# Optimization experiments

Measured on AMD Instinct MI355X. Metric: run time of the kernel, lower is better.

## Reference

```python
import jax, jax.numpy as jnp
import numpy as np

N_NODES = 50000
N_EDGES = 800000
H = 64  # n_hid


def _linear_params(key, fan_in, fan_out):
    lim = 1.0 / np.sqrt(fan_in)
    kw, kb = jax.random.split(key)
    w = jax.random.uniform(kw, (fan_in, fan_out), minval=-lim, maxval=lim, dtype=jnp.float32)
    b = jax.random.uniform(kb, (fan_out,), minval=-lim, maxval=lim, dtype=jnp.float32)
    return w, b


def setup_inputs() -> dict:
    key = jax.random.key(0)
    ks = jax.random.split(key, 10)
    nf_gc = jax.random.normal(ks[0], (N_NODES, H), dtype=jnp.float32)
    src = jax.random.randint(ks[1], (N_EDGES,), 0, N_NODES, dtype=jnp.int32)
    dst = jax.random.randint(ks[2], (N_EDGES,), 0, N_NODES, dtype=jnp.int32)
    res_w1, res_b1 = _linear_params(ks[3], H, H)
    res_w2, res_b2 = _linear_params(ks[4], H, H)
    lin1_w, lin1_b = _linear_params(ks[5], H, H)
    lin2_w, lin2_b = _linear_params(ks[6], H, H)
    msg_w1, msg_b1 = _linear_params(ks[7], 2 * H, 2 * H)
    msg_w2, msg_b2 = _linear_params(ks[8], 2 * H, 2 * H + 1)
    red_w, red_b = _linear_params(ks[9], 3 * H, H)
    return {
        'nf_gc': nf_gc, 'src': src, 'dst': dst,
        'res_w1': res_w1, 'res_b1': res_b1, 'res_w2': res_w2, 'res_b2': res_b2,
        'lin1_w': lin1_w, 'lin1_b': lin1_b, 'lin2_w': lin2_w, 'lin2_b': lin2_b,
        'msg_w1': msg_w1, 'msg_b1': msg_b1, 'msg_w2': msg_w2, 'msg_b2': msg_b2,
        'red_w': red_w, 'red_b': red_b,
    }


def reference(nf_gc, src, dst, res_w1, res_b1, res_w2, res_b2,
              lin1_w, lin1_b, lin2_w, lin2_b,
              msg_w1, msg_b1, msg_w2, msg_b2, red_w, red_b):
    n = nf_gc.shape[0]
    h = lin1_w.shape[0]
    # Residual block: lin2(lin1(x)) + x (no activation)
    x = ((nf_gc @ res_w1 + res_b1) @ res_w2 + res_b2) + nf_gc
    x1 = x @ lin1_w + lin1_b
    # Edge message: concat(src feat, dst feat) -> MLP(2h -> 2h -> 2h+1)
    e = jnp.concatenate([x[src], x[dst]], axis=1)          # [E, 2h]
    hmid = jax.nn.leaky_relu(e @ msg_w1 + msg_b1, 0.2)     # [E, 2h]
    o = hmid @ msg_w2 + msg_b2                             # [E, 2h+1]
    k = jax.nn.sigmoid(o[:, :1])
    f1 = o[:, 1:1 + h] * k
    f2 = o[:, 1 + h:] * k
    # Scatter-reduce: sum for f1, max for f2 (DGL gives 0 for isolated nodes)
    nfoc1 = jax.ops.segment_sum(f1, dst, num_segments=n)
    neg_inf = jnp.array(-jnp.inf, dtype=f2.dtype)
    nfoc2 = jnp.full((n, h), neg_inf, dtype=f2.dtype).at[dst].max(f2)
    deg = jnp.zeros((n,), dtype=f2.dtype).at[dst].add(1.0)
    nfoc2 = jnp.where(deg[:, None] > 0, nfoc2, 0.0)
    # Node reduce MLP (single linear 3h -> h), then outer lin2
    new_x = jnp.concatenate([x, nfoc1, nfoc2], axis=1) @ red_w + red_b
    x2 = new_x @ lin2_w + lin2_b
    return x1 + x2
```

## Files before the change

### kernel.cpp

```cpp
#include <hip/hip_runtime.h>

#define NN 50000
#define NE 800000

typedef _Float16 half8 __attribute__((ext_vector_type(8)));
typedef _Float16 half4 __attribute__((ext_vector_type(4)));
typedef float f32x4 __attribute__((ext_vector_type(4)));
typedef unsigned long long u64;

static const size_t XOFF   = 0;
static const size_t POFF   = 3200000;
static const size_t QOFF   = 6400000;
static const size_t N1OFF  = 9600000;
static const size_t N2OFF  = 12800000;
static const size_t W2TOFF = 16000000;
static const size_t WGHOFF = 16008192;
static const size_t RW1HOFF= 16008256;
static const size_t RW2HOFF= 16010304;
static const size_t L1WHOFF= 16012352;
static const size_t PWHOFF = 16014400;
static const size_t QWHOFF = 16018496;
static const size_t CNTOFF = 16022592;
static const size_t CUROFF = 16072592;
static const size_t PARTOFF= 16122592;
static const size_t SDOFF  = 16122848;

__device__ __forceinline__ unsigned fenc(float f){
  unsigned b = __float_as_uint(f);
  return (b & 0x80000000u) ? ~b : (b | 0x80000000u);
}
__device__ __forceinline__ float fdec(unsigned u){
  return (u & 0x80000000u) ? __uint_as_float(u & 0x7fffffffu) : __uint_as_float(~u);
}

__device__ __forceinline__ void gemm64(const float (*sIn)[65], const float* __restrict__ W,
                                       const float* __restrict__ bias, int t, float acc[4][4])
{
  const int c0 = (t & 15) * 4, r0 = (t >> 4) * 4;
  const float4 b4 = *(const float4*)&bias[c0];
  #pragma unroll
  for (int j = 0; j < 4; ++j){ acc[j][0]=b4.x; acc[j][1]=b4.y; acc[j][2]=b4.z; acc[j][3]=b4.w; }
  #pragma unroll 4
  for (int k = 0; k < 64; ++k){
    const float4 w4 = *(const float4*)&W[k*64 + c0];
    #pragma unroll
    for (int j = 0; j < 4; ++j){
      const float a = sIn[r0+j][k];
      acc[j][0] = fmaf(a, w4.x, acc[j][0]);
      acc[j][1] = fmaf(a, w4.y, acc[j][1]);
      acc[j][2] = fmaf(a, w4.z, acc[j][2]);
      acc[j][3] = fmaf(a, w4.w, acc[j][3]);
    }
  }
}

__device__ __forceinline__ int kperm(int kp){
  const int kg = kp >> 5, rem = kp & 31, kt = rem >> 2, j = rem & 3;
  return kt*16 + kg*4 + j;
}

__global__ __launch_bounds__(256) void prep_k(
    const float* __restrict__ w2, const float* __restrict__ rw1,
    const float* __restrict__ rw2, const float* __restrict__ l1w,
    const float* __restrict__ mw1,
    _Float16* __restrict__ w2t, _Float16* __restrict__ w2gh,
    _Float16* __restrict__ rw1h, _Float16* __restrict__ rw2h,
    _Float16* __restrict__ l1wh, _Float16* __restrict__ pwh,
    _Float16* __restrict__ qwh,
    const int* __restrict__ dst, unsigned* __restrict__ counts)
{
  const int b = blockIdx.x;
  if (b < 177){
    int i = b * 256 + threadIdx.x;
    if (i < 16384){
      int c = i >> 7, kp = i & 127;
      w2t[i] = (_Float16)w2[kperm(kp)*129 + 1 + c];
    } else if (i < 16512){
      int kp = i - 16384;
      w2gh[kp] = (_Float16)w2[kperm(kp)*129];
    } else if (i < 20608){
      int idx = i - 16512, c = idx >> 6, k = idx & 63;
      rw1h[idx] = (_Float16)rw1[k*64 + c];
    } else if (i < 24704){
      int idx = i - 20608, c = idx >> 6, k = idx & 63;
      rw2h[idx] = (_Float16)rw2[k*64 + c];
    } else if (i < 28800){
      int idx = i - 24704, c = idx >> 6, k = idx & 63;
      l1wh[idx] = (_Float16)l1w[k*64 + c];
    } else if (i < 36992){
      int idx = i - 28800, c = idx >> 6, k = idx & 63;
      pwh[idx] = (_Float16)mw1[k*128 + c];
    } else if (i < 45184){
      int idx = i - 36992, c = idx >> 6, k = idx & 63;
      qwh[idx] = (_Float16)mw1[(64 + k)*128 + c];
    }
  } else {
    int e = (b - 177) * 256 + threadIdx.x;
    if (e < NE) atomicAdd(&counts[dst[e]], 1u);
  }
}

__global__ __launch_bounds__(256) void scanA(const unsigned* __restrict__ counts,
                                             unsigned* __restrict__ partial)
{
  __shared__ unsigned s[256];
  const int t = threadIdx.x;
  const int idx = blockIdx.x * 256 + t;
  s[t] = (idx < NN) ? counts[idx] : 0u;
  __syncthreads();
  for (int d = 128; d > 0; d >>= 1){
    if (t < d) s[t] += s[t + d];
    __syncthreads();
  }
  if (t == 0) partial[blockIdx.x] = s[0];
}

__global__ __launch_bounds__(256) void scanB(unsigned* __restrict__ partial, int nb)
{
  __shared__ unsigned s[256];
  const int t = threadIdx.x;
  unsigned v = (t < nb) ? partial[t] : 0u;
  s[t] = v;
  __syncthreads();
  for (int d = 1; d < 256; d <<= 1){
    unsigned u = (t >= d) ? s[t - d] : 0u;
    __syncthreads();
    s[t] += u;
    __syncthreads();
  }
  if (t < nb) partial[t] = s[t] - v;
}

__global__ __launch_bounds__(256) void scanC(const unsigned* __restrict__ counts,
                                             const unsigned* __restrict__ partial,
                                             unsigned* __restrict__ cursor)
{
  __shared__ unsigned s[256];
  const int t = threadIdx.x;
  const int idx = blockIdx.x * 256 + t;
  unsigned v = (idx < NN) ? counts[idx] : 0u;
  s[t] = v;
  __syncthreads();
  for (int d = 1; d < 256; d <<= 1){
    unsigned u = (t >= d) ? s[t - d] : 0u;
    __syncthreads();
    s[t] += u;
    __syncthreads();
  }
  if (idx < NN) cursor[idx] = partial[blockIdx.x] + s[t] - v;
}

__global__ __launch_bounds__(256) void assign_k(const int* __restrict__ src,
                                                const int* __restrict__ dst,
                                                unsigned* __restrict__ cursor,
                                                u64* __restrict__ sdbuf)
{
  int e = blockIdx.x * 256 + threadIdx.x;
  if (e < NE){
    const int d = dst[e];
    unsigned slot = atomicAdd(&cursor[d], 1u);
    sdbuf[slot] = ((u64)(unsigned)d << 32) | (unsigned)src[e];
  }
}

__global__ __launch_bounds__(256) void node_pre_m(
    const float* __restrict__ nf,
    const _Float16* __restrict__ rw1h, const float* __restrict__ rb1,
    const _Float16* __restrict__ rw2h, const float* __restrict__ rb2,
    const _Float16* __restrict__ l1wh, const float* __restrict__ l1b,
    const _Float16* __restrict__ pwh, const _Float16* __restrict__ qwh,
    const float* __restrict__ mb1,
    float* __restrict__ x_out, _Float16* __restrict__ Pp, _Float16* __restrict__ Qp,
    float* __restrict__ out)
{
  __shared__ _Float16 sM[64][72];
  __shared__ _Float16 sT[64][72];
  const int t = threadIdx.x;
  const int lane = t & 63, wv = t >> 6;
  const int l15 = lane & 15, kg = lane >> 4;
  const int n0 = blockIdx.x * 64;

  {
    const int rr = t >> 4, c4 = (t & 15) * 4;
    #pragma unroll
    for (int i = 0; i < 4; ++i){
      int r = rr + i*16, n = n0 + r;
      float4 v = make_float4(0.f,0.f,0.f,0.f);
      if (n < NN) v = *(const float4*)&nf[(size_t)n*64 + c4];
      half4 h; h[0]=(_Float16)v.x; h[1]=(_Float16)v.y; h[2]=(_Float16)v.z; h[3]=(_Float16)v.w;
      *(half4*)&sM[r][c4] = h;
    }
  }
  __syncthreads();

  const int col = wv*16 + l15;

  {
    half4 bf[4];
    #pragma unroll
    for (int kt = 0; kt < 4; ++kt) bf[kt] = *(const half4*)&rw1h[col*64 + kt*16 + kg*4];
    const float bias = rb1[col];
    #pragma unroll
    for (int rt = 0; rt < 4; ++rt){
      f32x4 acc = {0.f,0.f,0.f,0.f};
      #pragma unroll
      for (int kt = 0; kt < 4; ++kt){
        const half4 af = *(const half4*)&sM[rt*16 + l15][kt*16 + kg*4];
        acc = __builtin_amdgcn_mfma_f32_16x16x16f16(af, bf[kt], acc, 0, 0, 0);
      }
      #pragma unroll
      for (int reg = 0; reg < 4; ++reg)
        sT[rt*16 + kg*4 + reg][col] = (_Float16)(acc[reg] + bias);
    }
  }
  __syncthreads();

  {
    half4 bf[4];
    #pragma unroll
    for (int kt = 0; kt < 4; ++kt) bf[kt] = *(const half4*)&rw2h[col*64 + kt*16 + kg*4];
    const float bias = rb2[col];
    #pragma unroll
    for (int rt = 0; rt < 4; ++rt){
      f32x4 acc = {0.f,0.f,0.f,0.f};
      #pragma unroll
      for (int kt = 0; kt < 4; ++kt){
        const half4 af = *(const half4*)&sT[rt*16 + l15][kt*16 + kg*4];
        acc = __builtin_amdgcn_mfma_f32_16x16x16f16(af, bf[kt], acc, 0, 0, 0);
      }
      #pragma unroll
      for (int reg = 0; reg < 4; ++reg){
        const int row = rt*16 + kg*4 + reg;
        const float xv = acc[reg] + bias + (float)sM[row][col];
        const int n = n0 + row;
        if (n < NN) x_out[(size_t)n*64 + col] = xv;
        sM[row][col] = (_Float16)xv;
      }
    }
  }
  __syncthreads();

  {
    half4 bf[4];
    #pragma unroll
    for (int kt = 0; kt < 4; ++kt) bf[kt] = *(const half4*)&l1wh[col*64 + kt*16 + kg*4];
    const float bias = l1b[col];
    #pragma unroll
    for (int rt = 0; rt < 4; ++rt){
      f32x4 acc = {0.f,0.f,0.f,0.f};
      #pragma unroll
      for (int kt = 0; kt < 4; ++kt){
        const half4 af = *(const half4*)&sM[rt*16 + l15][kt*16 + kg*4];
        acc = __builtin_amdgcn_mfma_f32_16x16x16f16(af, bf[kt], acc, 0, 0, 0);
      }
      #pragma unroll
      for (int reg = 0; reg < 4; ++reg){
        const int row = rt*16 + kg*4 + reg;
        const int n = n0 + row;
        if (n < NN) out[(size_t)n*64 + col] = acc[reg] + bias;
      }
    }
  }

  #pragma unroll
  for (int g = 0; g < 2; ++g){
    const _Float16* WH = g ? qwh : pwh;
    _Float16* dstp = g ? Qp : Pp;
    #pragma unroll
    for (int h = 0; h < 2; ++h){
      const int ct = h*4 + wv;
      const int colp = ct*16 + l15;
      half4 bf[4];
      #pragma unroll
      for (int kt = 0; kt < 4; ++kt) bf[kt] = *(const half4*)&WH[colp*64 + kt*16 + kg*4];
      const float bias = g ? 0.f : mb1[colp];
      const int kgc = l15 >> 2, jj = l15 & 3;
      const int pos = kgc*32 + ct*4 + jj;
      #pragma unroll
      for (int rt = 0; rt < 4; ++rt){
        f32x4 acc = {0.f,0.f,0.f,0.f};
        #pragma unroll
        for (int kt = 0; kt < 4; ++kt){
          const half4 af = *(const half4*)&sM[rt*16 + l15][kt*16 + kg*4];
          acc = __builtin_amdgcn_mfma_f32_16x16x16f16(af, bf[kt], acc, 0, 0, 0);
        }
        #pragma unroll
        for (int reg = 0; reg < 4; ++reg){
          const int row = rt*16 + kg*4 + reg;
          const int n = n0 + row;
          if (n < NN) dstp[(size_t)n*128 + pos] = (_Float16)(acc[reg] + bias);
        }
      }
    }
  }
}

__global__ __launch_bounds__(256) void edge_mlp8(
    const u64* __restrict__ sd,
    const _Float16* __restrict__ Pp, const _Float16* __restrict__ Qp,
    const _Float16* __restrict__ w2t, const _Float16* __restrict__ w2gh,
    const float* __restrict__ b2,
    float* __restrict__ nfoc1, unsigned* __restrict__ nfoc2)
{
  __shared__ _Float16 sA[64][136];
  __shared__ _Float16 sOutH[64][136];
  __shared__ float sK[2][64];
  __shared__ int   sD[2][64];
  const int t = threadIdx.x;
  const int lane = t & 63, wv = t >> 6;
  const int r  = lane & 15;
  const int kg = lane >> 4;
  const int row0 = wv * 16;
  const int base = blockIdx.x * 256;

  const int ct0 = wv * 2;
  half4 bf0[8], bf1[8];
  half8 wgr[4];
  float bias0, bias1;
  {
    const int col0 = ct0*16 + r, col1 = (ct0+1)*16 + r;
    bias0 = b2[1 + col0]; bias1 = b2[1 + col1];
    const _Float16* w0p = &w2t[(size_t)col0*128 + kg*32];
    const _Float16* w1p = &w2t[(size_t)col1*128 + kg*32];
    #pragma unroll
    for (int kt = 0; kt < 8; ++kt){
      bf0[kt] = *(const half4*)&w0p[kt*4];
      bf1[kt] = *(const half4*)&w1p[kt*4];
    }
    #pragma unroll
    for (int i = 0; i < 4; ++i) wgr[i] = *(const half8*)&w2gh[kg*32 + i*8];
  }
  const float gb = b2[0];

#define LOADRAW(PH, QH, SS, DD, TILE) { \
    const u64 sdv = sd[base + (TILE)*64 + row0 + r]; \
    SS = (int)(unsigned)(sdv & 0xffffffffu); \
    DD = (int)(unsigned)(sdv >> 32); \
    const _Float16* pr = &Pp[(size_t)SS * 128 + kg*32]; \
    const _Float16* qr = &Qp[(size_t)DD * 128 + kg*32]; \
    PH[0] = *(const half8*)&pr[0];  PH[1] = *(const half8*)&pr[8]; \
    PH[2] = *(const half8*)&pr[16]; PH[3] = *(const half8*)&pr[24]; \
    QH[0] = *(const half8*)&qr[0];  QH[1] = *(const half8*)&qr[8]; \
    QH[2] = *(const half8*)&qr[16]; QH[3] = *(const half8*)&qr[24]; }

#define PROCESS(PH, QH, DD, BUF) { \
    if (kg == 0) sD[BUF][row0 + r] = DD; \
    float gp = 0.f; \
    _Pragma("unroll") \
    for (int i = 0; i < 4; ++i){ \
      half8 mv = PH[i] + QH[i]; \
      const half8 m2 = mv * (_Float16)0.2f; \
      mv = __builtin_elementwise_max(mv, m2); \
      _Pragma("unroll") \
      for (int j = 0; j < 8; ++j) \
        gp = fmaf((float)mv[j], (float)wgr[i][j], gp); \
      *(half8*)&sA[row0 + r][kg*32 + i*8] = mv; \
    } \
    gp += __shfl_xor(gp, 16); \
    gp += __shfl_xor(gp, 32); \
    if (kg == 0) sK[BUF][row0 + r] = 1.f / (1.f + expf(-(gp + gb))); }

#define COMPUTE() { \
    _Pragma("unroll") \
    for (int rt = 0; rt < 4; ++rt){ \
      half4 af[8]; \
      const _Float16* ar = &sA[rt*16 + r][kg*32]; \
      _Pragma("unroll") \
      for (int kt = 0; kt < 8; ++kt) af[kt] = *(const half4*)&ar[kt*4]; \
      f32x4 a0 = {0.f,0.f,0.f,0.f}, a1 = {0.f,0.f,0.f,0.f}; \
      _Pragma("unroll") \
      for (int kt = 0; kt < 8; ++kt){ \
        a0 = __builtin_amdgcn_mfma_f32_16x16x16f16(af[kt], bf0[kt], a0, 0, 0, 0); \
        a1 = __builtin_amdgcn_mfma_f32_16x16x16f16(af[kt], bf1[kt], a1, 0, 0, 0); \
      } \
      _Pragma("unroll") \
      for (int reg = 0; reg < 4; ++reg){ \
        const int row = rt*16 + kg*4 + reg; \
        sOutH[row][ ct0   *16 + r] = (_Float16)(a0[reg] + bias0); \
        sOutH[row][(ct0+1)*16 + r] = (_Float16)(a1[reg] + bias1); \
      } \
    } }

#define REDUCE(BUF) { \
    const int c = t & 127; \
    const int rbeg = (t >> 7) * 32; \
    const bool isSum = c < 64; \
    float acc = isSum ? 0.f : -1e30f; \
    int curd = sD[BUF][rbeg]; \
    _Pragma("unroll 4") \
    for (int rw = rbeg; rw < rbeg + 32; ++rw){ \
      const float v = (float)sOutH[rw][c] * sK[BUF][rw]; \
      acc = isSum ? (acc + v) : fmaxf(acc, v); \
      const bool last = (rw == rbeg + 31) || (sD[BUF][rw + 1] != curd); \
      if (last){ \
        if (isSum){ \
          unsafeAtomicAdd(&nfoc1[(size_t)curd*64 + c], acc); \
          acc = 0.f; \
        } else { \
          atomicMax(&nfoc2[(size_t)curd*64 + (c - 64)], fenc(acc)); \
          acc = -1e30f; \
        } \
        if (rw < rbeg + 31) curd = sD[BUF][rw + 1]; \
      } \
    } }

  int s0, d0, s1, d1;
  half8 ph0[4], qh0[4], ph1[4], qh1[4];

  LOADRAW(ph0, qh0, s0, d0, 0);

  LOADRAW(ph1, qh1, s1, d1, 1);
  PROCESS(ph0, qh0, d0, 0);
  __syncthreads();
  COMPUTE();
  __syncthreads();
  REDUCE(0);

  LOADRAW(ph0, qh0, s0, d0, 2);
  PROCESS(ph1, qh1, d1, 1);
  __syncthreads();
  COMPUTE();
  __syncthreads();
  REDUCE(1);

  LOADRAW(ph1, qh1, s1, d1, 3);
  PROCESS(ph0, qh0, d0, 0);
  __syncthreads();
  COMPUTE();
  __syncthreads();
  REDUCE(0);

  PROCESS(ph1, qh1, d1, 1);
  __syncthreads();
  COMPUTE();
  __syncthreads();
  REDUCE(1);

#undef LOADRAW
#undef PROCESS
#undef COMPUTE
#undef REDUCE
}

__global__ __launch_bounds__(256) void node_post(
    const float* __restrict__ x, const float* __restrict__ nfoc1,
    const unsigned* __restrict__ nfoc2, const unsigned* __restrict__ counts,
    const float* __restrict__ redw, const float* __restrict__ redb,
    const float* __restrict__ l2w, const float* __restrict__ l2b,
    float* __restrict__ out)
{
  __shared__ float sC[64][197];
  __shared__ float sN[64][65];
  const int t = threadIdx.x;
  const int n0 = blockIdx.x * 64;
  const int rr = t >> 4, c4 = (t & 15) * 4;

  #pragma unroll
  for (int i = 0; i < 4; ++i){
    int r = rr + i*16, n = n0 + r;
    float4 xv = make_float4(0,0,0,0), f1 = make_float4(0,0,0,0);
    uint4 f2 = make_uint4(0,0,0,0);
    bool has = false;
    if (n < NN){
      xv = *(const float4*)&x[(size_t)n*64 + c4];
      f1 = *(const float4*)&nfoc1[(size_t)n*64 + c4];
      f2 = *(const uint4*)&nfoc2[(size_t)n*64 + c4];
      has = counts[n] > 0u;
    }
    sC[r][c4+0]=xv.x; sC[r][c4+1]=xv.y; sC[r][c4+2]=xv.z; sC[r][c4+3]=xv.w;
    sC[r][64+c4+0]=f1.x; sC[r][64+c4+1]=f1.y; sC[r][64+c4+2]=f1.z; sC[r][64+c4+3]=f1.w;
    sC[r][128+c4+0] = has ? fdec(f2.x) : 0.f;
    sC[r][128+c4+1] = has ? fdec(f2.y) : 0.f;
    sC[r][128+c4+2] = has ? fdec(f2.z) : 0.f;
    sC[r][128+c4+3] = has ? fdec(f2.w) : 0.f;
  }
  __syncthreads();

  const int c0 = (t & 15) * 4, r0 = (t >> 4) * 4;
  float acc[4][4];

  {
    const float4 b4 = *(const float4*)&redb[c0];
    #pragma unroll
    for (int j = 0; j < 4; ++j){ acc[j][0]=b4.x; acc[j][1]=b4.y; acc[j][2]=b4.z; acc[j][3]=b4.w; }
    #pragma unroll 4
    for (int k = 0; k < 192; ++k){
      const float4 w4 = *(const float4*)&redw[k*64 + c0];
      #pragma unroll
      for (int j = 0; j < 4; ++j){
        const float a = sC[r0+j][k];
        acc[j][0] = fmaf(a, w4.x, acc[j][0]);
        acc[j][1] = fmaf(a, w4.y, acc[j][1]);
        acc[j][2] = fmaf(a, w4.z, acc[j][2]);
        acc[j][3] = fmaf(a, w4.w, acc[j][3]);
      }
    }
    #pragma unroll
    for (int j = 0; j < 4; ++j)
      #pragma unroll
      for (int i = 0; i < 4; ++i) sN[r0+j][c0+i] = acc[j][i];
  }
  __syncthreads();

  gemm64(sN, l2w, l2b, t, acc);
  #pragma unroll
  for (int j = 0; j < 4; ++j){
    int n = n0 + r0 + j;
    if (n < NN){
      float4 cur = *(const float4*)&out[(size_t)n*64 + c0];
      cur.x += acc[j][0]; cur.y += acc[j][1]; cur.z += acc[j][2]; cur.w += acc[j][3];
      *(float4*)&out[(size_t)n*64 + c0] = cur;
    }
  }
}

extern "C" void kernel_launch(void* const* d_in, const int* in_sizes, int n_in,
                              void* d_out, int out_size, void* d_ws, size_t ws_size,
                              hipStream_t stream)
{
  const float* nf   = (const float*)d_in[0];
  const int*   src  = (const int*)d_in[1];
  const int*   dst  = (const int*)d_in[2];
  const float* rw1  = (const float*)d_in[3];
  const float* rb1  = (const float*)d_in[4];
  const float* rw2  = (const float*)d_in[5];
  const float* rb2  = (const float*)d_in[6];
  const float* l1w  = (const float*)d_in[7];
  const float* l1b  = (const float*)d_in[8];
  const float* l2w  = (const float*)d_in[9];
  const float* l2b  = (const float*)d_in[10];
  const float* mw1  = (const float*)d_in[11];
  const float* mb1  = (const float*)d_in[12];
  const float* mw2  = (const float*)d_in[13];
  const float* mb2  = (const float*)d_in[14];
  const float* redw = (const float*)d_in[15];
  const float* redb = (const float*)d_in[16];

  float* ws = (float*)d_ws;
  float*     x      = ws + XOFF;
  _Float16*  P      = (_Float16*)(ws + POFF);
  _Float16*  Q      = (_Float16*)(ws + QOFF);
  float*     nfoc1  = ws + N1OFF;
  unsigned*  nfoc2  = (unsigned*)(ws + N2OFF);
  _Float16*  w2t    = (_Float16*)(ws + W2TOFF);
  _Float16*  w2gh   = (_Float16*)(ws + WGHOFF);
  _Float16*  rw1h   = (_Float16*)(ws + RW1HOFF);
  _Float16*  rw2h   = (_Float16*)(ws + RW2HOFF);
  _Float16*  l1wh   = (_Float16*)(ws + L1WHOFF);
  _Float16*  pwh    = (_Float16*)(ws + PWHOFF);
  _Float16*  qwh    = (_Float16*)(ws + QWHOFF);
  unsigned*  counts = (unsigned*)(ws + CNTOFF);
  unsigned*  cursor = (unsigned*)(ws + CUROFF);
  unsigned*  partial= (unsigned*)(ws + PARTOFF);
  u64*       sdbuf  = (u64*)(ws + SDOFF);
  float*     out    = (float*)d_out;

  hipMemsetAsync(counts, 0, NN * sizeof(unsigned), stream);
  hipMemsetAsync(nfoc1, 0, (size_t)NN * 64 * 2 * sizeof(float), stream);
  hipLaunchKernelGGL(prep_k, dim3(177 + 3125), dim3(256), 0, stream,
                     mw2, rw1, rw2, l1w, mw1,
                     w2t, w2gh, rw1h, rw2h, l1wh, pwh, qwh, dst, counts);
  hipLaunchKernelGGL(scanA, dim3(196), dim3(256), 0, stream, counts, partial);
  hipLaunchKernelGGL(scanB, dim3(1),   dim3(256), 0, stream, partial, 196);
  hipLaunchKernelGGL(scanC, dim3(196), dim3(256), 0, stream, counts, partial, cursor);
  hipLaunchKernelGGL(assign_k, dim3(3125), dim3(256), 0, stream, src, dst, cursor, sdbuf);
  hipLaunchKernelGGL(node_pre_m, dim3(782), dim3(256), 0, stream,
                     nf, rw1h, rb1, rw2h, rb2, l1wh, l1b, pwh, qwh, mb1,
                     x, P, Q, out);
  hipLaunchKernelGGL(edge_mlp8, dim3(3125), dim3(256), 0, stream,
                     sdbuf, P, Q, w2t, w2gh, mb2, nfoc1, nfoc2);
  hipLaunchKernelGGL(node_post, dim3(782), dim3(256), 0, stream,
                     x, nfoc1, nfoc2, counts, redw, redb, l2w, l2b, out);
}
```

Measured before the change: 329.1 us.

## Fold reduce and lin2 weights into one matrix and run node_post on MFMA

Adds a one-block kernel that multiplies red_w by lin2_w (and folds the biases) into a single 192x64 fp16 weight. node_post is rewritten to do one fp16 MFMA GEMM over the concatenated [x, nfoc1, nfoc2] tile in place of two fp32 FMA GEMMs. x is now stored as fp16, which halves its write and read traffic. This removes FMA-bound node-side work but adds a serial single-block launch and lowers precision on x and the aggregates.

```diff
diff --git a/kernel.cpp b/kernel.cpp
--- a/kernel.cpp
+++ b/kernel.cpp
@@ -8,7 +8,7 @@
 typedef float f32x4 __attribute__((ext_vector_type(4)));
 typedef unsigned long long u64;
 
-static const size_t XOFF   = 0;
+static const size_t XHOFF  = 0;
 static const size_t POFF   = 3200000;
 static const size_t QOFF   = 6400000;
 static const size_t N1OFF  = 9600000;
@@ -24,6 +24,8 @@
 static const size_t CUROFF = 16072592;
 static const size_t PARTOFF= 16122592;
 static const size_t SDOFF  = 16122848;
+static const size_t FWOFF  = 17722848;
+static const size_t FBOFF  = 17729200;
 
 __device__ __forceinline__ unsigned fenc(float f){
   unsigned b = __float_as_uint(f);
@@ -31,27 +33,6 @@
 }
 __device__ __forceinline__ float fdec(unsigned u){
   return (u & 0x80000000u) ? __uint_as_float(u & 0x7fffffffu) : __uint_as_float(~u);
-}
-
-__device__ __forceinline__ void gemm64(const float (*sIn)[65], const float* __restrict__ W,
-                                       const float* __restrict__ bias, int t, float acc[4][4])
-{
-  const int c0 = (t & 15) * 4, r0 = (t >> 4) * 4;
-  const float4 b4 = *(const float4*)&bias[c0];
-  #pragma unroll
-  for (int j = 0; j < 4; ++j){ acc[j][0]=b4.x; acc[j][1]=b4.y; acc[j][2]=b4.z; acc[j][3]=b4.w; }
-  #pragma unroll 4
-  for (int k = 0; k < 64; ++k){
-    const float4 w4 = *(const float4*)&W[k*64 + c0];
-    #pragma unroll
-    for (int j = 0; j < 4; ++j){
-      const float a = sIn[r0+j][k];
-      acc[j][0] = fmaf(a, w4.x, acc[j][0]);
-      acc[j][1] = fmaf(a, w4.y, acc[j][1]);
-      acc[j][2] = fmaf(a, w4.z, acc[j][2]);
-      acc[j][3] = fmaf(a, w4.w, acc[j][3]);
-    }
-  }
 }
 
 __device__ __forceinline__ int kperm(int kp){
@@ -100,6 +81,35 @@
   }
 }
 
+__global__ __launch_bounds__(256) void fuse_k(
+    const float* __restrict__ redw, const float* __restrict__ redb,
+    const float* __restrict__ l2w, const float* __restrict__ l2b,
+    _Float16* __restrict__ fwh, float* __restrict__ fb)
+{
+  __shared__ float sl2[64][65];
+  const int t = threadIdx.x;
+  #pragma unroll
+  for (int i = 0; i < 16; ++i){
+    int idx = t*16 + i;
+    sl2[idx >> 6][idx & 63] = l2w[idx];
+  }
+  __syncthreads();
+  const int c = t & 63;
+  const int k0 = (t >> 6) * 48;
+  for (int k = k0; k < k0 + 48; ++k){
+    float a = 0.f;
+    #pragma unroll 8
+    for (int j = 0; j < 64; ++j) a = fmaf(redw[k*64 + j], sl2[j][c], a);
+    fwh[c*192 + k] = (_Float16)a;
+  }
+  if (t < 64){
+    float a = l2b[t];
+    #pragma unroll 8
+    for (int j = 0; j < 64; ++j) a = fmaf(redb[j], sl2[j][t], a);
+    fb[t] = a;
+  }
+}
+
 __global__ __launch_bounds__(256) void scanA(const unsigned* __restrict__ counts,
                                              unsigned* __restrict__ partial)
 {
@@ -170,7 +180,7 @@
     const _Float16* __restrict__ l1wh, const float* __restrict__ l1b,
     const _Float16* __restrict__ pwh, const _Float16* __restrict__ qwh,
     const float* __restrict__ mb1,
-    float* __restrict__ x_out, _Float16* __restrict__ Pp, _Float16* __restrict__ Qp,
+    _Float16* __restrict__ xh, _Float16* __restrict__ Pp, _Float16* __restrict__ Qp,
     float* __restrict__ out)
 {
   __shared__ _Float16 sM[64][72];
@@ -232,9 +242,10 @@
       for (int reg = 0; reg < 4; ++reg){
         const int row = rt*16 + kg*4 + reg;
         const float xv = acc[reg] + bias + (float)sM[row][col];
+        const _Float16 xvh = (_Float16)xv;
         const int n = n0 + row;
-        if (n < NN) x_out[(size_t)n*64 + col] = xv;
-        sM[row][col] = (_Float16)xv;
+        if (n < NN) xh[(size_t)n*64 + col] = xvh;
+        sM[row][col] = xvh;
       }
     }
   }
@@ -442,74 +453,65 @@
 #undef REDUCE
 }
 
-__global__ __launch_bounds__(256) void node_post(
-    const float* __restrict__ x, const float* __restrict__ nfoc1,
+__global__ __launch_bounds__(256) void node_post_m(
+    const _Float16* __restrict__ xh, const float* __restrict__ nfoc1,
     const unsigned* __restrict__ nfoc2, const unsigned* __restrict__ counts,
-    const float* __restrict__ redw, const float* __restrict__ redb,
-    const float* __restrict__ l2w, const float* __restrict__ l2b,
+    const _Float16* __restrict__ fwh, const float* __restrict__ fb,
     float* __restrict__ out)
 {
-  __shared__ float sC[64][197];
-  __shared__ float sN[64][65];
-  const int t = threadIdx.x;
+  __shared__ _Float16 sC[64][200];
+  const int t = threadIdx.x;
+  const int lane = t & 63, wv = t >> 6;
+  const int l15 = lane & 15, kg = lane >> 4;
   const int n0 = blockIdx.x * 64;
-  const int rr = t >> 4, c4 = (t & 15) * 4;
-
+
+  {
+    const int rr = t >> 4, c4 = (t & 15) * 4;
+    #pragma unroll
+    for (int i = 0; i < 4; ++i){
+      int r = rr + i*16, n = n0 + r;
+      half4 xv = {};
+      float4 f1 = make_float4(0,0,0,0);
+      uint4 f2 = make_uint4(0,0,0,0);
+      bool has = false;
+      if (n < NN){
+        xv = *(const half4*)&xh[(size_t)n*64 + c4];
+        f1 = *(const float4*)&nfoc1[(size_t)n*64 + c4];
+        f2 = *(const uint4*)&nfoc2[(size_t)n*64 + c4];
+        has = counts[n] > 0u;
+      }
+      *(half4*)&sC[r][c4] = xv;
+      half4 h1; h1[0]=(_Float16)f1.x; h1[1]=(_Float16)f1.y; h1[2]=(_Float16)f1.z; h1[3]=(_Float16)f1.w;
+      *(half4*)&sC[r][64 + c4] = h1;
+      half4 h2;
+      h2[0] = has ? (_Float16)fdec(f2.x) : (_Float16)0.f;
+      h2[1] = has ? (_Float16)fdec(f2.y) : (_Float16)0.f;
+      h2[2] = has ? (_Float16)fdec(f2.z) : (_Float16)0.f;
+      h2[3] = has ? (_Float16)fdec(f2.w) : (_Float16)0.f;
+      *(half4*)&sC[r][128 + c4] = h2;
+    }
+  }
+  __syncthreads();
+
+  const int col = wv*16 + l15;
+  half4 bf[12];
   #pragma unroll
-  for (int i = 0; i < 4; ++i){
-    int r = rr + i*16, n = n0 + r;
-    float4 xv = make_float4(0,0,0,0), f1 = make_float4(0,0,0,0);
-    uint4 f2 = make_uint4(0,0,0,0);
-    bool has = false;
-    if (n < NN){
-      xv = *(const float4*)&x[(size_t)n*64 + c4];
-      f1 = *(const float4*)&nfoc1[(size_t)n*64 + c4];
-      f2 = *(const uint4*)&nfoc2[(size_t)n*64 + c4];
-      has = counts[n] > 0u;
-    }
-    sC[r][c4+0]=xv.x; sC[r][c4+1]=xv.y; sC[r][c4+2]=xv.z; sC[r][c4+3]=xv.w;
-    sC[r][64+c4+0]=f1.x; sC[r][64+c4+1]=f1.y; sC[r][64+c4+2]=f1.z; sC[r][64+c4+3]=f1.w;
-    sC[r][128+c4+0] = has ? fdec(f2.x) : 0.f;
-    sC[r][128+c4+1] = has ? fdec(f2.y) : 0.f;
-    sC[r][128+c4+2] = has ? fdec(f2.z) : 0.f;
-    sC[r][128+c4+3] = has ? fdec(f2.w) : 0.f;
-  }
-  __syncthreads();
-
-  const int c0 = (t & 15) * 4, r0 = (t >> 4) * 4;
-  float acc[4][4];
-
-  {
-    const float4 b4 = *(const float4*)&redb[c0];
-    #pragma unroll
-    for (int j = 0; j < 4; ++j){ acc[j][0]=b4.x; acc[j][1]=b4.y; acc[j][2]=b4.z; acc[j][3]=b4.w; }
-    #pragma unroll 4
-    for (int k = 0; k < 192; ++k){
-      const float4 w4 = *(const float4*)&redw[k*64 + c0];
-      #pragma unroll
-      for (int j = 0; j < 4; ++j){
-        const float a = sC[r0+j][k];
-        acc[j][0] = fmaf(a, w4.x, acc[j][0]);
-        acc[j][1] = fmaf(a, w4.y, acc[j][1]);
-        acc[j][2] = fmaf(a, w4.z, acc[j][2]);
-        acc[j][3] = fmaf(a, w4.w, acc[j][3]);
-      }
-    }
-    #pragma unroll
-    for (int j = 0; j < 4; ++j)
-      #pragma unroll
-      for (int i = 0; i < 4; ++i) sN[r0+j][c0+i] = acc[j][i];
-  }
-  __syncthreads();
-
-  gemm64(sN, l2w, l2b, t, acc);
+  for (int kt = 0; kt < 12; ++kt) bf[kt] = *(const half4*)&fwh[col*192 + kt*16 + kg*4];
+  const float bias = fb[col];
+
   #pragma unroll
-  for (int j = 0; j < 4; ++j){
-    int n = n0 + r0 + j;
-    if (n < NN){
-      float4 cur = *(const float4*)&out[(size_t)n*64 + c0];
-      cur.x += acc[j][0]; cur.y += acc[j][1]; cur.z += acc[j][2]; cur.w += acc[j][3];
-      *(float4*)&out[(size_t)n*64 + c0] = cur;
+  for (int rt = 0; rt < 4; ++rt){
+    f32x4 acc = {0.f,0.f,0.f,0.f};
+    #pragma unroll
+    for (int kt = 0; kt < 12; ++kt){
+      const half4 af = *(const half4*)&sC[rt*16 + l15][kt*16 + kg*4];
+      acc = __builtin_amdgcn_mfma_f32_16x16x16f16(af, bf[kt], acc, 0, 0, 0);
+    }
+    #pragma unroll
+    for (int reg = 0; reg < 4; ++reg){
+      const int row = rt*16 + kg*4 + reg;
+      const int n = n0 + row;
+      if (n < NN) out[(size_t)n*64 + col] += acc[reg] + bias;
     }
   }
 }
@@ -537,7 +539,7 @@
   const float* redb = (const float*)d_in[16];
 
   float* ws = (float*)d_ws;
-  float*     x      = ws + XOFF;
+  _Float16*  xh     = (_Float16*)(ws + XHOFF);
   _Float16*  P      = (_Float16*)(ws + POFF);
   _Float16*  Q      = (_Float16*)(ws + QOFF);
   float*     nfoc1  = ws + N1OFF;
@@ -553,6 +555,8 @@
   unsigned*  cursor = (unsigned*)(ws + CUROFF);
   unsigned*  partial= (unsigned*)(ws + PARTOFF);
   u64*       sdbuf  = (u64*)(ws + SDOFF);
+  _Float16*  fwh    = (_Float16*)(ws + FWOFF);
+  float*     fb     = ws + FBOFF;
   float*     out    = (float*)d_out;
 
   hipMemsetAsync(counts, 0, NN * sizeof(unsigned), stream);
@@ -560,15 +564,16 @@
   hipLaunchKernelGGL(prep_k, dim3(177 + 3125), dim3(256), 0, stream,
                      mw2, rw1, rw2, l1w, mw1,
                      w2t, w2gh, rw1h, rw2h, l1wh, pwh, qwh, dst, counts);
+  hipLaunchKernelGGL(fuse_k, dim3(1), dim3(256), 0, stream, redw, redb, l2w, l2b, fwh, fb);
   hipLaunchKernelGGL(scanA, dim3(196), dim3(256), 0, stream, counts, partial);
   hipLaunchKernelGGL(scanB, dim3(1),   dim3(256), 0, stream, partial, 196);
   hipLaunchKernelGGL(scanC, dim3(196), dim3(256), 0, stream, counts, partial, cursor);
   hipLaunchKernelGGL(assign_k, dim3(3125), dim3(256), 0, stream, src, dst, cursor, sdbuf);
   hipLaunchKernelGGL(node_pre_m, dim3(782), dim3(256), 0, stream,
                      nf, rw1h, rb1, rw2h, rb2, l1wh, l1b, pwh, qwh, mb1,
-                     x, P, Q, out);
+                     xh, P, Q, out);
   hipLaunchKernelGGL(edge_mlp8, dim3(3125), dim3(256), 0, stream,
                      sdbuf, P, Q, w2t, w2gh, mb2, nfoc1, nfoc2);
-  hipLaunchKernelGGL(node_post, dim3(782), dim3(256), 0, stream,
-                     x, nfoc1, nfoc2, counts, redw, redb, l2w, l2b, out);
-}
+  hipLaunchKernelGGL(node_post_m, dim3(782), dim3(256), 0, stream,
+                     xh, nfoc1, nfoc2, counts, fwh, fb, out);
+}
```

Result: slower. 368.8 us (+12.1%).
